# Optimization experiments

Hardware: AMD Instinct MI355X
Metric: run time of the kernel (lower is better)

## Reference

```python
import jax, jax.numpy as jnp
import numpy as np

FACTOR = 5  # module default


def setup_inputs() -> dict:
    key = jax.random.key(0)
    k1, k2, k3, k4 = jax.random.split(key, 4)
    B, L, H, D = 4, 2048, 8, 64
    S = min(FACTOR * int(np.ceil(np.log(L))), L)  # sample_k = U_part = 40
    return {
        "queries": jax.random.normal(k1, (B, L, H, D), jnp.float32),
        "keys": jax.random.normal(k2, (B, L, H, D), jnp.float32),
        "values": jax.random.normal(k3, (B, L, H, D), jnp.float32),
        "index_sample": jax.random.randint(k4, (L, S), 0, L, jnp.int32),
    }


def reference(queries, keys, values, index_sample):
    # queries/keys/values: [B, L, H, D]; index_sample: [L_Q, sample_k]
    B, L_Q, H, D = queries.shape
    L_K = keys.shape[1]
    Q = jnp.transpose(queries, (0, 2, 1, 3))  # [B,H,L_Q,D]
    K = jnp.transpose(keys, (0, 2, 1, 3))     # [B,H,L_K,D]
    V = jnp.transpose(values, (0, 2, 1, 3))   # [B,H,L_V,D]

    u = min(FACTOR * int(np.ceil(np.log(L_Q))), L_Q)  # n_top

    # --- _prob_QK: sampled QK scores (gather instead of materializing K_expand) ---
    K_sample = K[:, :, index_sample, :]                       # [B,H,L_Q,S,D]
    QK_sample = jnp.einsum('bhld,bhlsd->bhls', Q, K_sample)   # [B,H,L_Q,S]
    M = QK_sample.max(-1) - QK_sample.sum(-1) / L_K           # sparsity measure [B,H,L_Q]
    M_top = jax.lax.top_k(M, u)[1]                            # [B,H,u] query indices

    Q_reduce = jnp.take_along_axis(Q, M_top[..., None], axis=2)  # [B,H,u,D]
    scale = 1.0 / np.sqrt(D)
    scores = jnp.einsum('bhud,bhkd->bhuk', Q_reduce, K) * scale  # [B,H,u,L_K]

    # --- initial context (mask_flag=True -> cumsum of V) ---
    context = jnp.cumsum(V, axis=2)                           # [B,H,L_Q,D]

    attn = jax.nn.softmax(scores, axis=-1)
    upd = jnp.einsum('bhuk,bhkd->bhud', attn, V)              # [B,H,u,D]

    bi = jnp.arange(B)[:, None, None]
    hi = jnp.arange(H)[None, :, None]
    context = context.at[bi, hi, M_top].set(upd)              # scatter selected rows

    return jnp.transpose(context, (0, 2, 1, 3))               # [B,L_Q,H,D]
```

## Files before the change

### kernel.cpp

```cpp
#include <hip/hip_runtime.h>

#define L_SEQ 2048
#define NH 8
#define DIM 64
#define SS 40
#define UU 40
#define NHD 512


__device__ __forceinline__ void m_body(const float* __restrict__ Qg,
                                       const float* __restrict__ Kg,
                                       const int* __restrict__ idx,
                                       float* __restrict__ M,
                                       int bx, int tid) {
    int lane = tid & 63;
    int b = bx & 3;
    int l = (bx >> 2) * 4 + (tid >> 6);
    int h = lane >> 3, c = lane & 7;

    const float* Qp = Qg + ((size_t)(b * L_SEQ + l) * NH + h) * DIM + c * 8;
    float4 q0 = *(const float4*)Qp;
    float4 q1 = *(const float4*)(Qp + 4);
    const float* Kbase = Kg + (size_t)b * L_SEQ * NHD + h * DIM + c * 8;
    const int* ip = idx + l * SS;

    float mx = -INFINITY, sm = 0.f;
#define DOT8(ka, kb, out) { \
    float d_ = ka.x * q0.x; \
    d_ = fmaf(ka.y, q0.y, d_); d_ = fmaf(ka.z, q0.z, d_); d_ = fmaf(ka.w, q0.w, d_); \
    d_ = fmaf(kb.x, q1.x, d_); d_ = fmaf(kb.y, q1.y, d_); \
    d_ = fmaf(kb.z, q1.z, d_); d_ = fmaf(kb.w, q1.w, d_); \
    d_ += __shfl_xor(d_, 1); d_ += __shfl_xor(d_, 2); d_ += __shfl_xor(d_, 4); \
    out = d_; }
    #pragma unroll
    for (int s = 0; s < SS; s += 5) {
        int k0 = ip[s], k1 = ip[s+1], k2 = ip[s+2], k3 = ip[s+3], k4 = ip[s+4];
        const float* r0 = Kbase + (size_t)k0 * NHD;
        const float* r1 = Kbase + (size_t)k1 * NHD;
        const float* r2 = Kbase + (size_t)k2 * NHD;
        const float* r3 = Kbase + (size_t)k3 * NHD;
        const float* r4 = Kbase + (size_t)k4 * NHD;
        float4 a0 = *(const float4*)r0, b0 = *(const float4*)(r0 + 4);
        float4 a1 = *(const float4*)r1, b1 = *(const float4*)(r1 + 4);
        float4 a2 = *(const float4*)r2, b2 = *(const float4*)(r2 + 4);
        float4 a3 = *(const float4*)r3, b3 = *(const float4*)(r3 + 4);
        float4 a4 = *(const float4*)r4, b4 = *(const float4*)(r4 + 4);
        float d0, d1, d2, d3, d4;
        DOT8(a0, b0, d0); DOT8(a1, b1, d1); DOT8(a2, b2, d2);
        DOT8(a3, b3, d3); DOT8(a4, b4, d4);
        mx = fmaxf(mx, fmaxf(fmaxf(d0, d1), fmaxf(fmaxf(d2, d3), d4)));
        sm += d0 + d1 + d2 + d3 + d4;
    }
#undef DOT8
    if (c == 0) M[((size_t)(b * NH + h)) * L_SEQ + l] = mx - sm * (1.0f / (float)L_SEQ);
}

__device__ __forceinline__ void csum8_body(const float* __restrict__ Vg,
                                           float* __restrict__ cs8,
                                           int wid, int lane) {
    int c8 = wid & 255, bh = wid >> 8;
    int b = bh >> 3, h = bh & 7;
    const float* Vp = Vg + ((size_t)(b * L_SEQ + c8 * 8) * NH + h) * DIM + lane;
    float s = 0.f;
    #pragma unroll
    for (int j = 0; j < 8; ++j) s += Vp[(size_t)j * NHD];
    cs8[((size_t)bh * 256 + c8) * 64 + lane] = s;
}

__device__ __forceinline__ void write8_body(const float* __restrict__ Vg,
                                            const float* __restrict__ cs8,
                                            float* __restrict__ out,
                                            int wid, int lane) {
    int c8 = wid & 255, bh = wid >> 8;
    int b = bh >> 3, h = bh & 7;
    float run = cs8[((size_t)bh * 256 + c8) * 64 + lane];
    size_t off = ((size_t)(b * L_SEQ + c8 * 8) * NH + h) * DIM + lane;
    const float* Vp = Vg + off;
    float* Op = out + off;
    #pragma unroll
    for (int j = 0; j < 8; ++j) {
        run += Vp[(size_t)j * NHD];
        Op[(size_t)j * NHD] = run;
    }
}

__device__ void attn_body(const float* __restrict__ Qg, const float* __restrict__ Kg,
                          const float* __restrict__ Vg, const int* __restrict__ Mtop,
                          float* __restrict__ pm, float* __restrict__ pl,
                          float* __restrict__ pO, float* __restrict__ out,
                          int nsplit, int direct, int bx, int tid,
                          float* qs, float* ks, float* ps,
                          float* mm, float* ll, float* al) {
    int bh = bx / nsplit, sp = bx - bh * nsplit;
    int b = bh >> 3, h = bh & 7;
    int cpb = 32 / nsplit;
    const int* mt = Mtop + bh * UU;

    for (int i = tid; i < UU * DIM / 8; i += 256) {
        int u = i >> 3, dv = (i & 7) * 8;
        int row = mt[u];
        const float* qp = Qg + ((size_t)(b * L_SEQ + row) * NH + h) * DIM + dv;
        *(float4*)&qs[u * DIM + dv]     = *(const float4*)qp;
        *(float4*)&qs[u * DIM + dv + 4] = *(const float4*)(qp + 4);
    }
    if (tid < UU) { mm[tid] = -INFINITY; ll[tid] = 0.f; }

    int d0 = (tid & 31) * 2, ugp = tid >> 5;
    float o0[5], o1[5];
    #pragma unroll
    for (int j = 0; j < 5; ++j) { o0[j] = 0.f; o1[j] = 0.f; }

    for (int c = 0; c < cpb; ++c) {
        int k0 = (sp * cpb + c) * 64;
        if (c) __syncthreads();
        for (int i = tid; i < 64 * DIM / 8; i += 256) {
            int r = i >> 3, dv = (i & 7) * 8;
            const float* kp = Kg + ((size_t)(b * L_SEQ + k0 + r) * NH + h) * DIM + dv;
            *(float4*)&ks[r * 68 + dv]     = *(const float4*)kp;
            *(float4*)&ks[r * 68 + dv + 4] = *(const float4*)(kp + 4);
        }
        __syncthreads();

        {
            int k = tid & 63, ug = tid >> 6;
            float acc[10];
            #pragma unroll
            for (int j = 0; j < 10; ++j) acc[j] = 0.f;
            for (int d = 0; d < DIM; d += 4) {
                float4 kv = *(float4*)&ks[k * 68 + d];
                #pragma unroll
                for (int j = 0; j < 10; ++j) {
                    float4 qv = *(float4*)&qs[(ug * 10 + j) * DIM + d];
                    acc[j] = fmaf(qv.x, kv.x, acc[j]);
                    acc[j] = fmaf(qv.y, kv.y, acc[j]);
                    acc[j] = fmaf(qv.z, kv.z, acc[j]);
                    acc[j] = fmaf(qv.w, kv.w, acc[j]);
                }
            }
            #pragma unroll
            for (int j = 0; j < 10; ++j) ps[(ug * 10 + j) * 68 + k] = acc[j] * 0.125f;
        }
        __syncthreads();

        for (int i = tid; i < 64 * DIM / 8; i += 256) {
            int r = i >> 3, dv = (i & 7) * 8;
            const float* vp = Vg + ((size_t)(b * L_SEQ + k0 + r) * NH + h) * DIM + dv;
            *(float4*)&ks[r * 68 + dv]     = *(const float4*)vp;
            *(float4*)&ks[r * 68 + dv + 4] = *(const float4*)(vp + 4);
        }
        if (tid < UU) {
            float mc = -INFINITY;
            for (int k = 0; k < 64; ++k) mc = fmaxf(mc, ps[tid * 68 + k]);
            float mn = fmaxf(mm[tid], mc);
            float a = __expf(mm[tid] - mn);
            float s = 0.f;
            for (int k = 0; k < 64; ++k) {
                float e = __expf(ps[tid * 68 + k] - mn);
                ps[tid * 68 + k] = e;
                s += e;
            }
            ll[tid] = ll[tid] * a + s;
            mm[tid] = mn;
            al[tid] = a;
        }
        __syncthreads();

        {
            #pragma unroll
            for (int j = 0; j < 5; ++j) {
                float a = al[ugp * 5 + j];
                o0[j] *= a; o1[j] *= a;
            }
            for (int k = 0; k < 64; k += 4) {
                float vf0[4], vf1[4];
                #pragma unroll
                for (int kk = 0; kk < 4; ++kk) {
                    float2 vv = *(float2*)&ks[(k + kk) * 68 + d0];
                    vf0[kk] = vv.x;
                    vf1[kk] = vv.y;
                }
                #pragma unroll
                for (int j = 0; j < 5; ++j) {
                    float4 pv = *(float4*)&ps[(ugp * 5 + j) * 68 + k];
                    o0[j] = fmaf(pv.x, vf0[0], o0[j]); o1[j] = fmaf(pv.x, vf1[0], o1[j]);
                    o0[j] = fmaf(pv.y, vf0[1], o0[j]); o1[j] = fmaf(pv.y, vf1[1], o1[j]);
                    o0[j] = fmaf(pv.z, vf0[2], o0[j]); o1[j] = fmaf(pv.z, vf1[2], o1[j]);
                    o0[j] = fmaf(pv.w, vf0[3], o0[j]); o1[j] = fmaf(pv.w, vf1[3], o1[j]);
                }
            }
        }
    }

    if (!direct) {
        if (tid < UU) {
            pm[((size_t)bh * nsplit + sp) * UU + tid] = mm[tid];
            pl[((size_t)bh * nsplit + sp) * UU + tid] = ll[tid];
        }
        size_t basep = ((size_t)bh * nsplit + sp) * UU * DIM;
        #pragma unroll
        for (int j = 0; j < 5; ++j) {
            *(float2*)&pO[basep + (size_t)(ugp * 5 + j) * DIM + d0] = make_float2(o0[j], o1[j]);
        }
    } else {
        #pragma unroll
        for (int j = 0; j < 5; ++j) {
            int u = ugp * 5 + j;
            int row = mt[u];
            float inv = 1.0f / ll[u];
            size_t o = ((size_t)(b * L_SEQ + row) * NH + h) * DIM + d0;
            out[o]     = o0[j] * inv;
            out[o + 1] = o1[j] * inv;
        }
    }
}


__global__ __launch_bounds__(256) void stage1_kernel(const float* __restrict__ Qg,
                                                     const float* __restrict__ Kg,
                                                     const int* __restrict__ idx,
                                                     const float* __restrict__ Vg,
                                                     float* __restrict__ M,
                                                     float* __restrict__ cs8) {
    int bx = blockIdx.x, tid = threadIdx.x;
    if (bx < 2048) {
        m_body(Qg, Kg, idx, M, bx, tid);
    } else {
        int wid = (bx - 2048) * 4 + (tid >> 6);
        csum8_body(Vg, cs8, wid, tid & 63);
    }
}

__global__ __launch_bounds__(256) void stage2_kernel(const float* __restrict__ M,
                                                     int* __restrict__ Mtop,
                                                     float* __restrict__ cs8) {
    __shared__ unsigned hist[256];
    __shared__ unsigned suf[256];
    __shared__ int eq_list[64];
    __shared__ unsigned sh_bin, sh_need, sh_cnt, sh_eqc;
    __shared__ float buf[256 * 64];
    int bx = blockIdx.x, tid = threadIdx.x;

    if (bx < 32) {
        int bh = bx;
        const float* Mrow = M + (size_t)bh * L_SEQ;
        int base = tid * 8;
        float4 a0 = *(const float4*)(Mrow + base);
        float4 a1 = *(const float4*)(Mrow + base + 4);
        float fv[8] = {a0.x, a0.y, a0.z, a0.w, a1.x, a1.y, a1.z, a1.w};
        unsigned key[8];
        #pragma unroll
        for (int j = 0; j < 8; ++j) {
            unsigned u = __float_as_uint(fv[j]);
            key[j] = (u & 0x80000000u) ? ~u : (u | 0x80000000u);
        }
        unsigned actmask = 0xffu;
        unsigned thresh = 0;
        int need = UU;
        #pragma unroll
        for (int shift = 24; shift >= 0; shift -= 8) {
            hist[tid] = 0;
            __syncthreads();
            #pragma unroll
            for (int j = 0; j < 8; ++j)
                if ((actmask >> j) & 1u)
                    atomicAdd(&hist[(key[j] >> shift) & 0xffu], 1u);
            __syncthreads();
            if (tid < 64) {
                int b0 = tid * 4;
                unsigned h0 = hist[b0], h1 = hist[b0 + 1], h2 = hist[b0 + 2], h3 = hist[b0 + 3];
                unsigned loc = h0 + h1 + h2 + h3;
                unsigned s = loc;
                #pragma unroll
                for (int off = 1; off < 64; off <<= 1) {
                    unsigned o = __shfl_down(s, off, 64);
                    if (tid + off < 64) s += o;
                }
                unsigned tail = s - loc;
                suf[b0 + 3] = tail;
                suf[b0 + 2] = tail + h3;
                suf[b0 + 1] = tail + h3 + h2;
                suf[b0 + 0] = tail + h3 + h2 + h1;
            }
            __syncthreads();
            {
                int sb = (int)suf[tid];
                if (sb < need && sb + (int)hist[tid] >= need) {
                    sh_bin = (unsigned)tid;
                    sh_need = (unsigned)(need - sb);
                }
            }
            __syncthreads();
            unsigned Bb = sh_bin;
            need = (int)sh_need;
            thresh = (thresh << 8) | Bb;
            #pragma unroll
            for (int j = 0; j < 8; ++j)
                if ((actmask >> j) & 1u)
                    if (((key[j] >> shift) & 0xffu) != Bb) actmask &= ~(1u << j);
            __syncthreads();
        }
        if (tid == 0) { sh_cnt = 0; sh_eqc = 0; }
        __syncthreads();
        int* op = Mtop + bh * UU;
        #pragma unroll
        for (int j = 0; j < 8; ++j) {
            if (key[j] > thresh) {
                unsigned p = atomicAdd(&sh_cnt, 1u);
                op[p] = base + j;
            } else if (key[j] == thresh) {
                unsigned p = atomicAdd(&sh_eqc, 1u);
                if (p < 64) eq_list[p] = base + j;
            }
        }
        __syncthreads();
        unsigned cnt = sh_cnt, eqc = sh_eqc;
        if ((int)eqc == need) {
            if (tid < (unsigned)need) op[cnt + tid] = eq_list[tid];
        } else if (tid == 0) {
            if (eqc <= 64u) {
                for (int t = 0; t < need; ++t) {
                    int mi = t;
                    for (int j = t + 1; j < (int)eqc; ++j)
                        if (eq_list[j] < eq_list[mi]) mi = j;
                    int tmp = eq_list[t]; eq_list[t] = eq_list[mi]; eq_list[mi] = tmp;
                    op[cnt + t] = eq_list[t];
                }
            } else {
                int taken = 0;
                for (int i = 0; i < L_SEQ && taken < need; ++i) {
                    unsigned u = __float_as_uint(Mrow[i]);
                    unsigned k = (u & 0x80000000u) ? ~u : (u | 0x80000000u);
                    if (k == thresh) op[cnt + taken++] = i;
                }
            }
        }
    } else {
        int bh = bx - 32;
        float* g = cs8 + (size_t)bh * 16384;
        for (int it = 0; it < 16; ++it) {
            int i = it * 1024 + tid * 4;
            *(float4*)&buf[i] = *(const float4*)&g[i];
        }
        __syncthreads();
        if (tid < 64) {
            float run = 0.f;
            for (int c = 0; c < 256; ++c) {
                float t = buf[c * 64 + tid];
                buf[c * 64 + tid] = run;
                run += t;
            }
        }
        __syncthreads();
        for (int it = 0; it < 16; ++it) {
            int i = it * 1024 + tid * 4;
            *(float4*)&g[i] = *(const float4*)&buf[i];
        }
    }
}

__global__ __launch_bounds__(256) void stage3_kernel(const float* __restrict__ Qg,
                                                     const float* __restrict__ Kg,
                                                     const float* __restrict__ Vg,
                                                     const int* __restrict__ Mtop,
                                                     const float* __restrict__ cs8,
                                                     float* __restrict__ pm,
                                                     float* __restrict__ pl,
                                                     float* __restrict__ pO,
                                                     float* __restrict__ out,
                                                     int nattn, int nsplit) {
    __shared__ float qs[UU * DIM];
    __shared__ float ks[64 * 68];
    __shared__ float ps[UU * 68];
    __shared__ float mm[UU], ll[UU], al[UU];
    int bx = blockIdx.x, tid = threadIdx.x;
    if (bx < nattn) {
        attn_body(Qg, Kg, Vg, Mtop, pm, pl, pO, out, nsplit, 0, bx, tid,
                  qs, ks, ps, mm, ll, al);
    } else {
        int wid = (bx - nattn) * 4 + (tid >> 6);
        write8_body(Vg, cs8, out, wid, tid & 63);
    }
}

__global__ __launch_bounds__(256) void attn_kernel(const float* __restrict__ Qg,
                                                   const float* __restrict__ Kg,
                                                   const float* __restrict__ Vg,
                                                   const int* __restrict__ Mtop,
                                                   float* __restrict__ pm,
                                                   float* __restrict__ pl,
                                                   float* __restrict__ pO,
                                                   float* __restrict__ out,
                                                   int nsplit, int direct) {
    __shared__ float qs[UU * DIM];
    __shared__ float ks[64 * 68];
    __shared__ float ps[UU * 68];
    __shared__ float mm[UU], ll[UU], al[UU];
    attn_body(Qg, Kg, Vg, Mtop, pm, pl, pO, out, nsplit, direct,
              blockIdx.x, threadIdx.x, qs, ks, ps, mm, ll, al);
}

__global__ __launch_bounds__(256) void combine_kernel(const float* __restrict__ pm,
                                                      const float* __restrict__ pl,
                                                      const float* __restrict__ pO,
                                                      const int* __restrict__ Mtop,
                                                      float* __restrict__ out, int nsplit) {
    int wid = blockIdx.x * 4 + (threadIdx.x >> 6);
    int lane = threadIdx.x & 63;
    int u = wid % UU;
    int bh = wid / UU;
    int b = bh >> 3, h = bh & 7;
    float mg = -INFINITY;
    for (int c = 0; c < nsplit; ++c) mg = fmaxf(mg, pm[((size_t)bh * nsplit + c) * UU + u]);
    float acc = 0.f, lsum = 0.f;
    for (int c = 0; c < nsplit; ++c) {
        size_t pb = ((size_t)bh * nsplit + c) * UU + u;
        float w = __expf(pm[pb] - mg);
        lsum = fmaf(pl[pb], w, lsum);
        acc = fmaf(w, pO[pb * DIM + lane], acc);
    }
    int row = Mtop[bh * UU + u];
    out[((size_t)(b * L_SEQ + row) * NH + h) * DIM + lane] = acc / lsum;
}

__global__ __launch_bounds__(256) void csum_fused_kernel(const float* __restrict__ Vg,
                                                         float* __restrict__ out) {
    __shared__ float css[32 * 64];
    int bh = blockIdx.x, tid = threadIdx.x;
    int b = bh >> 3, h = bh & 7;
    int cc = tid >> 3, d8 = (tid & 7) * 8;
    size_t off = ((size_t)(b * L_SEQ + cc * 64) * NH + h) * DIM + d8;
    const float* Vp = Vg + off;
    float s[8];
    #pragma unroll
    for (int j = 0; j < 8; ++j) s[j] = 0.f;
    for (int l = 0; l < 64; ++l) {
        float4 r0 = *(const float4*)(Vp + (size_t)l * NHD);
        float4 r1 = *(const float4*)(Vp + (size_t)l * NHD + 4);
        s[0] += r0.x; s[1] += r0.y; s[2] += r0.z; s[3] += r0.w;
        s[4] += r1.x; s[5] += r1.y; s[6] += r1.z; s[7] += r1.w;
    }
    #pragma unroll
    for (int j = 0; j < 8; ++j) css[cc * 64 + d8 + j] = s[j];
    __syncthreads();
    if (tid < 64) {
        float run = 0.f;
        for (int c = 0; c < 32; ++c) {
            float t = css[c * 64 + tid];
            css[c * 64 + tid] = run;
            run += t;
        }
    }
    __syncthreads();
    float r8[8];
    #pragma unroll
    for (int j = 0; j < 8; ++j) r8[j] = css[cc * 64 + d8 + j];
    float* Op = out + off;
    for (int l = 0; l < 64; ++l) {
        float4 r0 = *(const float4*)(Vp + (size_t)l * NHD);
        float4 r1 = *(const float4*)(Vp + (size_t)l * NHD + 4);
        r8[0] += r0.x; r8[1] += r0.y; r8[2] += r0.z; r8[3] += r0.w;
        r8[4] += r1.x; r8[5] += r1.y; r8[6] += r1.z; r8[7] += r1.w;
        *(float4*)(Op + (size_t)l * NHD)     = make_float4(r8[0], r8[1], r8[2], r8[3]);
        *(float4*)(Op + (size_t)l * NHD + 4) = make_float4(r8[4], r8[5], r8[6], r8[7]);
    }
}

extern "C" void kernel_launch(void* const* d_in, const int* in_sizes, int n_in,
                              void* d_out, int out_size, void* d_ws, size_t ws_size,
                              hipStream_t stream) {
    const float* Q = (const float*)d_in[0];
    const float* K = (const float*)d_in[1];
    const float* V = (const float*)d_in[2];
    const int* idx = (const int*)d_in[3];
    float* out = (float*)d_out;
    float* wsf = (float*)d_ws;

    int n = 0;
    const int cands[5] = {32, 16, 8, 4, 2};
    for (int i = 0; i < 5; ++i) {
        size_t need = (size_t)(591104 + 84480 * cands[i]) * 4;
        if (ws_size >= need) { n = cands[i]; break; }
    }

    if (n > 0) {
        float* M    = wsf;
        int*   Mtop = (int*)(wsf + 65536);
        float* pm   = wsf + 66816;
        float* pl   = pm + 1280 * (size_t)n;
        float* pO   = pl + 1280 * (size_t)n;
        float* cs8  = pO + 81920 * (size_t)n;
        stage1_kernel<<<4096, 256, 0, stream>>>(Q, K, idx, V, M, cs8);
        stage2_kernel<<<64, 256, 0, stream>>>(M, Mtop, cs8);
        stage3_kernel<<<32 * n + 2048, 256, 0, stream>>>(Q, K, V, Mtop, cs8,
                                                         pm, pl, pO, out, 32 * n, n);
        combine_kernel<<<320, 256, 0, stream>>>(pm, pl, pO, Mtop, out, n);
    } else if (ws_size >= (size_t)(66816 + 524288) * 4) {
        float* M    = wsf;
        int*   Mtop = (int*)(wsf + 65536);
        float* cs8  = wsf + 66816;
        stage1_kernel<<<4096, 256, 0, stream>>>(Q, K, idx, V, M, cs8);
        stage2_kernel<<<64, 256, 0, stream>>>(M, Mtop, cs8);
        stage3_kernel<<<2048, 256, 0, stream>>>(Q, K, V, Mtop, cs8,
                                                nullptr, nullptr, nullptr, out, 0, 1);
        attn_kernel<<<32, 256, 0, stream>>>(Q, K, V, Mtop, nullptr, nullptr, nullptr,
                                            out, 1, 1);
    } else {
        float* M    = (float*)d_out;
        int*   Mtop = (int*)d_ws;
        stage1_kernel<<<2048, 256, 0, stream>>>(Q, K, idx, nullptr, M, nullptr);
        stage2_kernel<<<32, 256, 0, stream>>>(M, Mtop, nullptr);
        csum_fused_kernel<<<32, 256, 0, stream>>>(V, out);
        attn_kernel<<<32, 256, 0, stream>>>(Q, K, V, Mtop, nullptr, nullptr, nullptr,
                                            out, 1, 1);
    }
}
```

Measured before the change: 177.7 us.

## Stage sampled K rows into LDS with whole-row coalesced loads; fix split count

The sparsity-measure stage now has each wavefront load 10 full sampled K rows (all heads, 2 KB each) into LDS at a time, using global_load_lds when available, then reads the per-head slices from LDS for the dot products. The goal is to replace many small scattered 32-byte per-lane gathers with contiguous row loads. The cost is an 80 KB shared buffer per block, which lowers occupancy and also affects the csum blocks in the same kernel, plus a full wait barrier per batch of rows. The launcher also fixes the key-split count at 8 instead of taking the largest one that fits the workspace.

```diff
diff --git a/kernel.cpp b/kernel.cpp
--- a/kernel.cpp
+++ b/kernel.cpp
@@ -7,51 +7,68 @@
 #define UU 40
 #define NHD 512
 
+#if defined(__has_builtin)
+#  if __has_builtin(__builtin_amdgcn_global_load_lds)
+#    define HAVE_GLDS 1
+#  endif
+#endif
+
+#ifdef HAVE_GLDS
+#define GLDS16(gp, lp) __builtin_amdgcn_global_load_lds( \
+    (const __attribute__((address_space(1))) void*)(gp), \
+    (__attribute__((address_space(3))) void*)(lp), 16, 0, 0)
+#endif
+
 
 __device__ __forceinline__ void m_body(const float* __restrict__ Qg,
                                        const float* __restrict__ Kg,
                                        const int* __restrict__ idx,
                                        float* __restrict__ M,
-                                       int bx, int tid) {
-    int lane = tid & 63;
+                                       int bx, int tid, float* ksm) {
+    int w = tid >> 6, lane = tid & 63;
     int b = bx & 3;
-    int l = (bx >> 2) * 4 + (tid >> 6);
+    int l = (bx >> 2) * 4 + w;
     int h = lane >> 3, c = lane & 7;
+    float* kw = ksm + w * 5120;
 
     const float* Qp = Qg + ((size_t)(b * L_SEQ + l) * NH + h) * DIM + c * 8;
     float4 q0 = *(const float4*)Qp;
     float4 q1 = *(const float4*)(Qp + 4);
-    const float* Kbase = Kg + (size_t)b * L_SEQ * NHD + h * DIM + c * 8;
-    const int* ip = idx + l * SS;
+    int kidx = idx[l * SS + (lane < SS ? lane : 0)];
+    const float* Kb = Kg + (size_t)b * L_SEQ * NHD;
 
     float mx = -INFINITY, sm = 0.f;
-#define DOT8(ka, kb, out) { \
-    float d_ = ka.x * q0.x; \
-    d_ = fmaf(ka.y, q0.y, d_); d_ = fmaf(ka.z, q0.z, d_); d_ = fmaf(ka.w, q0.w, d_); \
-    d_ = fmaf(kb.x, q1.x, d_); d_ = fmaf(kb.y, q1.y, d_); \
-    d_ = fmaf(kb.z, q1.z, d_); d_ = fmaf(kb.w, q1.w, d_); \
-    d_ += __shfl_xor(d_, 1); d_ += __shfl_xor(d_, 2); d_ += __shfl_xor(d_, 4); \
-    out = d_; }
-    #pragma unroll
-    for (int s = 0; s < SS; s += 5) {
-        int k0 = ip[s], k1 = ip[s+1], k2 = ip[s+2], k3 = ip[s+3], k4 = ip[s+4];
-        const float* r0 = Kbase + (size_t)k0 * NHD;
-        const float* r1 = Kbase + (size_t)k1 * NHD;
-        const float* r2 = Kbase + (size_t)k2 * NHD;
-        const float* r3 = Kbase + (size_t)k3 * NHD;
-        const float* r4 = Kbase + (size_t)k4 * NHD;
-        float4 a0 = *(const float4*)r0, b0 = *(const float4*)(r0 + 4);
-        float4 a1 = *(const float4*)r1, b1 = *(const float4*)(r1 + 4);
-        float4 a2 = *(const float4*)r2, b2 = *(const float4*)(r2 + 4);
-        float4 a3 = *(const float4*)r3, b3 = *(const float4*)(r3 + 4);
-        float4 a4 = *(const float4*)r4, b4 = *(const float4*)(r4 + 4);
-        float d0, d1, d2, d3, d4;
-        DOT8(a0, b0, d0); DOT8(a1, b1, d1); DOT8(a2, b2, d2);
-        DOT8(a3, b3, d3); DOT8(a4, b4, d4);
-        mx = fmaxf(mx, fmaxf(fmaxf(d0, d1), fmaxf(fmaxf(d2, d3), d4)));
-        sm += d0 + d1 + d2 + d3 + d4;
-    }
-#undef DOT8
+    for (int sb = 0; sb < 4; ++sb) {
+        #pragma unroll
+        for (int j = 0; j < 10; ++j) {
+            int ki = __shfl(kidx, sb * 10 + j);
+            const float* g = Kb + (size_t)ki * NHD;
+#ifdef HAVE_GLDS
+            GLDS16(g + lane * 4, kw + j * 512);
+            GLDS16(g + 256 + lane * 4, kw + j * 512 + 256);
+#else
+            *(float4*)(kw + j * 512 + lane * 4)       = *(const float4*)(g + lane * 4);
+            *(float4*)(kw + j * 512 + 256 + lane * 4) = *(const float4*)(g + 256 + lane * 4);
+#endif
+        }
+        asm volatile("s_waitcnt vmcnt(0) lgkmcnt(0)" ::: "memory");
+        #pragma unroll
+        for (int j = 0; j < 10; ++j) {
+            const float* src = kw + j * 512 + lane * 8;
+            float4 ka = *(const float4*)src;
+            float4 kb = *(const float4*)(src + 4);
+            float d_ = ka.x * q0.x;
+            d_ = fmaf(ka.y, q0.y, d_); d_ = fmaf(ka.z, q0.z, d_); d_ = fmaf(ka.w, q0.w, d_);
+            d_ = fmaf(kb.x, q1.x, d_); d_ = fmaf(kb.y, q1.y, d_);
+            d_ = fmaf(kb.z, q1.z, d_); d_ = fmaf(kb.w, q1.w, d_);
+            d_ += __shfl_xor(d_, 1);
+            d_ += __shfl_xor(d_, 2);
+            d_ += __shfl_xor(d_, 4);
+            mx = fmaxf(mx, d_);
+            sm += d_;
+        }
+        asm volatile("s_waitcnt lgkmcnt(0)" ::: "memory");
+    }
     if (c == 0) M[((size_t)(b * NH + h)) * L_SEQ + l] = mx - sm * (1.0f / (float)L_SEQ);
 }
 
@@ -221,9 +238,10 @@
                                                      const float* __restrict__ Vg,
                                                      float* __restrict__ M,
                                                      float* __restrict__ cs8) {
+    __shared__ float ksm[4 * 5120];
     int bx = blockIdx.x, tid = threadIdx.x;
     if (bx < 2048) {
-        m_body(Qg, Kg, idx, M, bx, tid);
+        m_body(Qg, Kg, idx, M, bx, tid, ksm);
     } else {
         int wid = (bx - 2048) * 4 + (tid >> 6);
         csum8_body(Vg, cs8, wid, tid & 63);
@@ -475,14 +493,10 @@
     float* out = (float*)d_out;
     float* wsf = (float*)d_ws;
 
-    int n = 0;
-    const int cands[5] = {32, 16, 8, 4, 2};
-    for (int i = 0; i < 5; ++i) {
-        size_t need = (size_t)(591104 + 84480 * cands[i]) * 4;
-        if (ws_size >= need) { n = cands[i]; break; }
-    }
-
-    if (n > 0) {
+    const int n = 8;
+    size_t need_full = (size_t)(65536 + 1280 + 1280 * n * 2 + 81920 * n + 524288) * 4;
+
+    if (ws_size >= need_full) {
         float* M    = wsf;
         int*   Mtop = (int*)(wsf + 65536);
         float* pm   = wsf + 66816;
```

New measurement: 180.2 us. No clear change (+1.4%).

## Fuse four stage kernels into one cooperative persistent kernel with grid syncs

Applied to the files above, without the earlier changes.

Replaces the four separate launches (M scoring plus chunk sums, top-k plus prefix, attention plus cumsum write, split combine) with a single cooperative kernel of 1024 blocks that loops over the old block work and separates stages with grid.sync. The goal is to remove inter-kernel launch gaps and tail effects. The split count is fixed at 8 rather than picked from workspace size, the prefix pass is processed in two halves to shrink shared memory, and shared arrays are carved from one buffer. In exchange it depends on cooperative launch support, on 1024 blocks being co-resident, and on grid-wide barriers, and it falls back to the multi-kernel path if the launch fails.

```diff
diff --git a/kernel.cpp b/kernel.cpp
--- a/kernel.cpp
+++ b/kernel.cpp
@@ -1,4 +1,7 @@
 #include <hip/hip_runtime.h>
+#include <hip/hip_cooperative_groups.h>
+
+namespace cg = cooperative_groups;
 
 #define L_SEQ 2048
 #define NH 8
@@ -13,9 +16,9 @@
                                        const int* __restrict__ idx,
                                        float* __restrict__ M,
                                        int bx, int tid) {
-    int lane = tid & 63;
+    int w = tid >> 6, lane = tid & 63;
     int b = bx & 3;
-    int l = (bx >> 2) * 4 + (tid >> 6);
+    int l = (bx >> 2) * 4 + w;
     int h = lane >> 3, c = lane & 7;
 
     const float* Qp = Qg + ((size_t)(b * L_SEQ + l) * NH + h) * DIM + c * 8;
@@ -84,6 +87,133 @@
     }
 }
 
+__device__ void topk_body(const float* __restrict__ M, int* __restrict__ Mtop,
+                          int bh, int tid, float* smemf) {
+    unsigned* hist = (unsigned*)smemf;
+    unsigned* suf  = hist + 256;
+    int* eq_list   = (int*)(suf + 256);
+    unsigned* scal = (unsigned*)(eq_list + 64);
+    const float* Mrow = M + (size_t)bh * L_SEQ;
+    int base = tid * 8;
+
+    float4 a0 = *(const float4*)(Mrow + base);
+    float4 a1 = *(const float4*)(Mrow + base + 4);
+    float fv[8] = {a0.x, a0.y, a0.z, a0.w, a1.x, a1.y, a1.z, a1.w};
+    unsigned key[8];
+    #pragma unroll
+    for (int j = 0; j < 8; ++j) {
+        unsigned u = __float_as_uint(fv[j]);
+        key[j] = (u & 0x80000000u) ? ~u : (u | 0x80000000u);
+    }
+    unsigned actmask = 0xffu, thresh = 0;
+    int need = UU;
+    #pragma unroll
+    for (int shift = 24; shift >= 0; shift -= 8) {
+        hist[tid] = 0;
+        __syncthreads();
+        #pragma unroll
+        for (int j = 0; j < 8; ++j)
+            if ((actmask >> j) & 1u)
+                atomicAdd(&hist[(key[j] >> shift) & 0xffu], 1u);
+        __syncthreads();
+        if (tid < 64) {
+            int b0 = tid * 4;
+            unsigned h0 = hist[b0], h1 = hist[b0 + 1], h2 = hist[b0 + 2], h3 = hist[b0 + 3];
+            unsigned loc = h0 + h1 + h2 + h3;
+            unsigned s = loc;
+            #pragma unroll
+            for (int off = 1; off < 64; off <<= 1) {
+                unsigned o = __shfl_down(s, off, 64);
+                if (tid + off < 64) s += o;
+            }
+            unsigned tail = s - loc;
+            suf[b0 + 3] = tail;
+            suf[b0 + 2] = tail + h3;
+            suf[b0 + 1] = tail + h3 + h2;
+            suf[b0 + 0] = tail + h3 + h2 + h1;
+        }
+        __syncthreads();
+        {
+            int sb = (int)suf[tid];
+            if (sb < need && sb + (int)hist[tid] >= need) {
+                scal[0] = (unsigned)tid;
+                scal[1] = (unsigned)(need - sb);
+            }
+        }
+        __syncthreads();
+        unsigned Bb = scal[0];
+        need = (int)scal[1];
+        thresh = (thresh << 8) | Bb;
+        #pragma unroll
+        for (int j = 0; j < 8; ++j)
+            if ((actmask >> j) & 1u)
+                if (((key[j] >> shift) & 0xffu) != Bb) actmask &= ~(1u << j);
+        __syncthreads();
+    }
+    if (tid == 0) { scal[2] = 0; scal[3] = 0; }
+    __syncthreads();
+    int* op = Mtop + bh * UU;
+    #pragma unroll
+    for (int j = 0; j < 8; ++j) {
+        if (key[j] > thresh) {
+            unsigned p = atomicAdd(&scal[2], 1u);
+            op[p] = base + j;
+        } else if (key[j] == thresh) {
+            unsigned p = atomicAdd(&scal[3], 1u);
+            if (p < 64) eq_list[p] = base + j;
+        }
+    }
+    __syncthreads();
+    unsigned cnt = scal[2], eqc = scal[3];
+    if ((int)eqc == need) {
+        if (tid < (unsigned)need) op[cnt + tid] = eq_list[tid];
+    } else if (tid == 0) {
+        if (eqc <= 64u) {
+            for (int t = 0; t < need; ++t) {
+                int mi = t;
+                for (int j = t + 1; j < (int)eqc; ++j)
+                    if (eq_list[j] < eq_list[mi]) mi = j;
+                int tmp = eq_list[t]; eq_list[t] = eq_list[mi]; eq_list[mi] = tmp;
+                op[cnt + t] = eq_list[t];
+            }
+        } else {
+            int taken = 0;
+            for (int i = 0; i < L_SEQ && taken < need; ++i) {
+                unsigned u = __float_as_uint(Mrow[i]);
+                unsigned k = (u & 0x80000000u) ? ~u : (u | 0x80000000u);
+                if (k == thresh) op[cnt + taken++] = i;
+            }
+        }
+    }
+    __syncthreads();
+}
+
+__device__ void prefix_body(float* __restrict__ cs8, int bh, int tid, float* buf) {
+    float* g = cs8 + (size_t)bh * 16384;
+    float run = 0.f;
+    for (int half = 0; half < 2; ++half) {
+        float* gh = g + half * 8192;
+        for (int it = 0; it < 8; ++it) {
+            int i = it * 1024 + tid * 4;
+            *(float4*)&buf[i] = *(const float4*)&gh[i];
+        }
+        __syncthreads();
+        if (tid < 64) {
+            for (int c = 0; c < 128; ++c) {
+                float t = buf[c * 64 + tid];
+                buf[c * 64 + tid] = run;
+                run += t;
+            }
+        }
+        __syncthreads();
+        for (int it = 0; it < 8; ++it) {
+            int i = it * 1024 + tid * 4;
+            *(float4*)&gh[i] = *(const float4*)&buf[i];
+        }
+        __syncthreads();
+    }
+}
+
 __device__ void attn_body(const float* __restrict__ Qg, const float* __restrict__ Kg,
                           const float* __restrict__ Vg, const int* __restrict__ Mtop,
                           float* __restrict__ pm, float* __restrict__ pl,
@@ -120,7 +250,6 @@
             *(float4*)&ks[r * 68 + dv + 4] = *(const float4*)(kp + 4);
         }
         __syncthreads();
-
         {
             int k = tid & 63, ug = tid >> 6;
             float acc[10];
@@ -141,7 +270,6 @@
             for (int j = 0; j < 10; ++j) ps[(ug * 10 + j) * 68 + k] = acc[j] * 0.125f;
         }
         __syncthreads();
-
         for (int i = tid; i < 64 * DIM / 8; i += 256) {
             int r = i >> 3, dv = (i & 7) * 8;
             const float* vp = Vg + ((size_t)(b * L_SEQ + k0 + r) * NH + h) * DIM + dv;
@@ -164,7 +292,6 @@
             al[tid] = a;
         }
         __syncthreads();
-
         {
             #pragma unroll
             for (int j = 0; j < 5; ++j) {
@@ -214,6 +341,77 @@
     }
 }
 
+__device__ __forceinline__ void combine_body(const float* __restrict__ pm,
+                                             const float* __restrict__ pl,
+                                             const float* __restrict__ pO,
+                                             const int* __restrict__ Mtop,
+                                             float* __restrict__ out, int nsplit,
+                                             int wid, int lane) {
+    int u = wid % UU;
+    int bh = wid / UU;
+    int b = bh >> 3, h = bh & 7;
+    float mg = -INFINITY;
+    for (int c = 0; c < nsplit; ++c) mg = fmaxf(mg, pm[((size_t)bh * nsplit + c) * UU + u]);
+    float acc = 0.f, lsum = 0.f;
+    for (int c = 0; c < nsplit; ++c) {
+        size_t pb = ((size_t)bh * nsplit + c) * UU + u;
+        float w = __expf(pm[pb] - mg);
+        lsum = fmaf(pl[pb], w, lsum);
+        acc = fmaf(w, pO[pb * DIM + lane], acc);
+    }
+    int row = Mtop[bh * UU + u];
+    out[((size_t)(b * L_SEQ + row) * NH + h) * DIM + lane] = acc / lsum;
+}
+
+#define NSPLIT 8
+__global__ __launch_bounds__(256, 4) void mono_kernel(
+    const float* __restrict__ Qg, const float* __restrict__ Kg,
+    const float* __restrict__ Vg, const int* __restrict__ idx,
+    float* __restrict__ M, int* __restrict__ Mtop,
+    float* __restrict__ pm, float* __restrict__ pl, float* __restrict__ pO,
+    float* __restrict__ cs8, float* __restrict__ out) {
+    __shared__ float smem[9752];
+    cg::grid_group grid = cg::this_grid();
+    int bx = blockIdx.x, tid = threadIdx.x;
+
+    #pragma unroll
+    for (int i = 0; i < 4; ++i) {
+        int v = bx + 1024 * i;
+        if (v < 2048) {
+            m_body(Qg, Kg, idx, M, v, tid);
+        } else {
+            int wid = (v - 2048) * 4 + (tid >> 6);
+            csum8_body(Vg, cs8, wid, tid & 63);
+        }
+    }
+    grid.sync();
+
+    if (bx < 32) topk_body(M, Mtop, bx, tid, smem);
+    else if (bx < 64) prefix_body(cs8, bx - 32, tid, smem);
+    grid.sync();
+
+    if (bx < 32 * NSPLIT) {
+        attn_body(Qg, Kg, Vg, Mtop, pm, pl, pO, out, NSPLIT, 0, bx, tid,
+                  smem, smem + 2560, smem + 6912,
+                  smem + 9632, smem + 9672, smem + 9712);
+    } else {
+        #pragma unroll
+        for (int i = 0; i < 3; ++i) {
+            int v = (bx - 256) + 768 * i;
+            if (v < 2048) {
+                int wid = v * 4 + (tid >> 6);
+                write8_body(Vg, cs8, out, wid, tid & 63);
+            }
+        }
+    }
+    grid.sync();
+
+    if (bx < 320) {
+        int wid = bx * 4 + (tid >> 6);
+        combine_body(pm, pl, pO, Mtop, out, NSPLIT, wid, tid & 63);
+    }
+}
+
 
 __global__ __launch_bounds__(256) void stage1_kernel(const float* __restrict__ Qg,
                                                      const float* __restrict__ Kg,
@@ -233,129 +431,10 @@
 __global__ __launch_bounds__(256) void stage2_kernel(const float* __restrict__ M,
                                                      int* __restrict__ Mtop,
                                                      float* __restrict__ cs8) {
-    __shared__ unsigned hist[256];
-    __shared__ unsigned suf[256];
-    __shared__ int eq_list[64];
-    __shared__ unsigned sh_bin, sh_need, sh_cnt, sh_eqc;
-    __shared__ float buf[256 * 64];
+    __shared__ float sbuf[8192];
     int bx = blockIdx.x, tid = threadIdx.x;
-
-    if (bx < 32) {
-        int bh = bx;
-        const float* Mrow = M + (size_t)bh * L_SEQ;
-        int base = tid * 8;
-        float4 a0 = *(const float4*)(Mrow + base);
-        float4 a1 = *(const float4*)(Mrow + base + 4);
-        float fv[8] = {a0.x, a0.y, a0.z, a0.w, a1.x, a1.y, a1.z, a1.w};
-        unsigned key[8];
-        #pragma unroll
-        for (int j = 0; j < 8; ++j) {
-            unsigned u = __float_as_uint(fv[j]);
-            key[j] = (u & 0x80000000u) ? ~u : (u | 0x80000000u);
-        }
-        unsigned actmask = 0xffu;
-        unsigned thresh = 0;
-        int need = UU;
-        #pragma unroll
-        for (int shift = 24; shift >= 0; shift -= 8) {
-            hist[tid] = 0;
-            __syncthreads();
-            #pragma unroll
-            for (int j = 0; j < 8; ++j)
-                if ((actmask >> j) & 1u)
-                    atomicAdd(&hist[(key[j] >> shift) & 0xffu], 1u);
-            __syncthreads();
-            if (tid < 64) {
-                int b0 = tid * 4;
-                unsigned h0 = hist[b0], h1 = hist[b0 + 1], h2 = hist[b0 + 2], h3 = hist[b0 + 3];
-                unsigned loc = h0 + h1 + h2 + h3;
-                unsigned s = loc;
-                #pragma unroll
-                for (int off = 1; off < 64; off <<= 1) {
-                    unsigned o = __shfl_down(s, off, 64);
-                    if (tid + off < 64) s += o;
-                }
-                unsigned tail = s - loc;
-                suf[b0 + 3] = tail;
-                suf[b0 + 2] = tail + h3;
-                suf[b0 + 1] = tail + h3 + h2;
-                suf[b0 + 0] = tail + h3 + h2 + h1;
-            }
-            __syncthreads();
-            {
-                int sb = (int)suf[tid];
-                if (sb < need && sb + (int)hist[tid] >= need) {
-                    sh_bin = (unsigned)tid;
-                    sh_need = (unsigned)(need - sb);
-                }
-            }
-            __syncthreads();
-            unsigned Bb = sh_bin;
-            need = (int)sh_need;
-            thresh = (thresh << 8) | Bb;
-            #pragma unroll
-            for (int j = 0; j < 8; ++j)
-                if ((actmask >> j) & 1u)
-                    if (((key[j] >> shift) & 0xffu) != Bb) actmask &= ~(1u << j);
-            __syncthreads();
-        }
-        if (tid == 0) { sh_cnt = 0; sh_eqc = 0; }
-        __syncthreads();
-        int* op = Mtop + bh * UU;
-        #pragma unroll
-        for (int j = 0; j < 8; ++j) {
-            if (key[j] > thresh) {
-                unsigned p = atomicAdd(&sh_cnt, 1u);
-                op[p] = base + j;
-            } else if (key[j] == thresh) {
-                unsigned p = atomicAdd(&sh_eqc, 1u);
-                if (p < 64) eq_list[p] = base + j;
-            }
-        }
-        __syncthreads();
-        unsigned cnt = sh_cnt, eqc = sh_eqc;
-        if ((int)eqc == need) {
-            if (tid < (unsigned)need) op[cnt + tid] = eq_list[tid];
-        } else if (tid == 0) {
-            if (eqc <= 64u) {
-                for (int t = 0; t < need; ++t) {
-                    int mi = t;
-                    for (int j = t + 1; j < (int)eqc; ++j)
-                        if (eq_list[j] < eq_list[mi]) mi = j;
-                    int tmp = eq_list[t]; eq_list[t] = eq_list[mi]; eq_list[mi] = tmp;
-                    op[cnt + t] = eq_list[t];
-                }
-            } else {
-                int taken = 0;
-                for (int i = 0; i < L_SEQ && taken < need; ++i) {
-                    unsigned u = __float_as_uint(Mrow[i]);
-                    unsigned k = (u & 0x80000000u) ? ~u : (u | 0x80000000u);
-                    if (k == thresh) op[cnt + taken++] = i;
-                }
-            }
-        }
-    } else {
-        int bh = bx - 32;
-        float* g = cs8 + (size_t)bh * 16384;
-        for (int it = 0; it < 16; ++it) {
-            int i = it * 1024 + tid * 4;
-            *(float4*)&buf[i] = *(const float4*)&g[i];
-        }
-        __syncthreads();
-        if (tid < 64) {
-            float run = 0.f;
-            for (int c = 0; c < 256; ++c) {
-                float t = buf[c * 64 + tid];
-                buf[c * 64 + tid] = run;
-                run += t;
-            }
-        }
-        __syncthreads();
-        for (int it = 0; it < 16; ++it) {
-            int i = it * 1024 + tid * 4;
-            *(float4*)&g[i] = *(const float4*)&buf[i];
-        }
-    }
+    if (bx < 32) topk_body(M, Mtop, bx, tid, sbuf);
+    else prefix_body(cs8, bx - 32, tid, sbuf);
 }
 
 __global__ __launch_bounds__(256) void stage3_kernel(const float* __restrict__ Qg,
@@ -368,14 +447,12 @@
                                                      float* __restrict__ pO,
                                                      float* __restrict__ out,
                                                      int nattn, int nsplit) {
-    __shared__ float qs[UU * DIM];
-    __shared__ float ks[64 * 68];
-    __shared__ float ps[UU * 68];
-    __shared__ float mm[UU], ll[UU], al[UU];
+    __shared__ float smem[9752];
     int bx = blockIdx.x, tid = threadIdx.x;
     if (bx < nattn) {
         attn_body(Qg, Kg, Vg, Mtop, pm, pl, pO, out, nsplit, 0, bx, tid,
-                  qs, ks, ps, mm, ll, al);
+                  smem, smem + 2560, smem + 6912,
+                  smem + 9632, smem + 9672, smem + 9712);
     } else {
         int wid = (bx - nattn) * 4 + (tid >> 6);
         write8_body(Vg, cs8, out, wid, tid & 63);
@@ -386,17 +463,12 @@
                                                    const float* __restrict__ Kg,
                                                    const float* __restrict__ Vg,
                                                    const int* __restrict__ Mtop,
-                                                   float* __restrict__ pm,
-                                                   float* __restrict__ pl,
-                                                   float* __restrict__ pO,
-                                                   float* __restrict__ out,
-                                                   int nsplit, int direct) {
-    __shared__ float qs[UU * DIM];
-    __shared__ float ks[64 * 68];
-    __shared__ float ps[UU * 68];
-    __shared__ float mm[UU], ll[UU], al[UU];
-    attn_body(Qg, Kg, Vg, Mtop, pm, pl, pO, out, nsplit, direct,
-              blockIdx.x, threadIdx.x, qs, ks, ps, mm, ll, al);
+                                                   float* __restrict__ out) {
+    __shared__ float smem[9752];
+    attn_body(Qg, Kg, Vg, Mtop, nullptr, nullptr, nullptr, out, 1, 1,
+              blockIdx.x, threadIdx.x,
+              smem, smem + 2560, smem + 6912,
+              smem + 9632, smem + 9672, smem + 9712);
 }
 
 __global__ __launch_bounds__(256) void combine_kernel(const float* __restrict__ pm,
@@ -405,21 +477,7 @@
                                                       const int* __restrict__ Mtop,
                                                       float* __restrict__ out, int nsplit) {
     int wid = blockIdx.x * 4 + (threadIdx.x >> 6);
-    int lane = threadIdx.x & 63;
-    int u = wid % UU;
-    int bh = wid / UU;
-    int b = bh >> 3, h = bh & 7;
-    float mg = -INFINITY;
-    for (int c = 0; c < nsplit; ++c) mg = fmaxf(mg, pm[((size_t)bh * nsplit + c) * UU + u]);
-    float acc = 0.f, lsum = 0.f;
-    for (int c = 0; c < nsplit; ++c) {
-        size_t pb = ((size_t)bh * nsplit + c) * UU + u;
-        float w = __expf(pm[pb] - mg);
-        lsum = fmaf(pl[pb], w, lsum);
-        acc = fmaf(w, pO[pb * DIM + lane], acc);
-    }
-    int row = Mtop[bh * UU + u];
-    out[((size_t)(b * L_SEQ + row) * NH + h) * DIM + lane] = acc / lsum;
+    combine_body(pm, pl, pO, Mtop, out, nsplit, wid, threadIdx.x & 63);
 }
 
 __global__ __launch_bounds__(256) void csum_fused_kernel(const float* __restrict__ Vg,
@@ -475,42 +533,41 @@
     float* out = (float*)d_out;
     float* wsf = (float*)d_ws;
 
-    int n = 0;
-    const int cands[5] = {32, 16, 8, 4, 2};
-    for (int i = 0; i < 5; ++i) {
-        size_t need = (size_t)(591104 + 84480 * cands[i]) * 4;
-        if (ws_size >= need) { n = cands[i]; break; }
-    }
-
-    if (n > 0) {
+    const int n = NSPLIT;
+    size_t need_full = (size_t)(65536 + 1280 + 1280 * n * 2 + 81920 * n + 524288) * 4;
+
+    if (ws_size >= need_full) {
         float* M    = wsf;
         int*   Mtop = (int*)(wsf + 65536);
         float* pm   = wsf + 66816;
         float* pl   = pm + 1280 * (size_t)n;
         float* pO   = pl + 1280 * (size_t)n;
         float* cs8  = pO + 81920 * (size_t)n;
-        stage1_kernel<<<4096, 256, 0, stream>>>(Q, K, idx, V, M, cs8);
-        stage2_kernel<<<64, 256, 0, stream>>>(M, Mtop, cs8);
-        stage3_kernel<<<32 * n + 2048, 256, 0, stream>>>(Q, K, V, Mtop, cs8,
-                                                         pm, pl, pO, out, 32 * n, n);
-        combine_kernel<<<320, 256, 0, stream>>>(pm, pl, pO, Mtop, out, n);
-    } else if (ws_size >= (size_t)(66816 + 524288) * 4) {
-        float* M    = wsf;
-        int*   Mtop = (int*)(wsf + 65536);
-        float* cs8  = wsf + 66816;
-        stage1_kernel<<<4096, 256, 0, stream>>>(Q, K, idx, V, M, cs8);
-        stage2_kernel<<<64, 256, 0, stream>>>(M, Mtop, cs8);
-        stage3_kernel<<<2048, 256, 0, stream>>>(Q, K, V, Mtop, cs8,
-                                                nullptr, nullptr, nullptr, out, 0, 1);
-        attn_kernel<<<32, 256, 0, stream>>>(Q, K, V, Mtop, nullptr, nullptr, nullptr,
-                                            out, 1, 1);
+
+        int coop = 0, dev = 0;
+        hipGetDevice(&dev);
+        hipDeviceGetAttribute(&coop, hipDeviceAttributeCooperativeLaunch, dev);
+        hipError_t e = hipErrorUnknown;
+        if (coop) {
+            void* args[] = {(void*)&Q, (void*)&K, (void*)&V, (void*)&idx,
+                            (void*)&M, (void*)&Mtop, (void*)&pm, (void*)&pl,
+                            (void*)&pO, (void*)&cs8, (void*)&out};
+            e = hipLaunchCooperativeKernel((void*)mono_kernel, dim3(1024), dim3(256),
+                                           args, 0, stream);
+        }
+        if (e != hipSuccess) {
+            stage1_kernel<<<4096, 256, 0, stream>>>(Q, K, idx, V, M, cs8);
+            stage2_kernel<<<64, 256, 0, stream>>>(M, Mtop, cs8);
+            stage3_kernel<<<32 * n + 2048, 256, 0, stream>>>(Q, K, V, Mtop, cs8,
+                                                             pm, pl, pO, out, 32 * n, n);
+            combine_kernel<<<320, 256, 0, stream>>>(pm, pl, pO, Mtop, out, n);
+        }
     } else {
         float* M    = (float*)d_out;
         int*   Mtop = (int*)d_ws;
         stage1_kernel<<<2048, 256, 0, stream>>>(Q, K, idx, nullptr, M, nullptr);
         stage2_kernel<<<32, 256, 0, stream>>>(M, Mtop, nullptr);
         csum_fused_kernel<<<32, 256, 0, stream>>>(V, out);
-        attn_kernel<<<32, 256, 0, stream>>>(Q, K, V, Mtop, nullptr, nullptr, nullptr,
-                                            out, 1, 1);
-    }
-}
+        attn_kernel<<<32, 256, 0, stream>>>(Q, K, V, Mtop, out);
+    }
+}
```

Result: slower. 550.6 us (+209.9%).
